# Kernel optimization log

Hardware: AMD Instinct MI355X
Metric: run time of the kernel (lower is better)

Reference implementation:

```python
import jax, jax.numpy as jnp
import numpy as np

NEG_BIG = -9e15  # matches torch's -9000000000000000.0 mask value


def _l2norm(x, eps=1e-12):
    # F.normalize(x, p=2, dim=1)
    n = jnp.sqrt(jnp.sum(x * x, axis=1, keepdims=True))
    return x / jnp.maximum(n, eps)


def _fusion_attribute(emb, att_emb, adj):
    # cosine similarity [N, M]
    sim = _l2norm(emb) @ _l2norm(att_emb).T
    sim = sim * adj
    # masked softmax over dim=1: zeros -> -9e15
    logits = jnp.where(sim != 0, sim, jnp.full_like(sim, NEG_BIG))
    attention = jax.nn.softmax(logits, axis=1)
    return attention @ att_emb


def setup_inputs() -> dict:
    key = jax.random.key(0)
    k1, k2, k3, k4 = jax.random.split(key, 4)
    U, I, D = 10000, 8000, 64
    users_emb = 0.1 * jax.random.normal(k1, (U, D), dtype=jnp.float32)  # init.normal_(std=0.1)
    items_emb = 0.1 * jax.random.normal(k2, (I, D), dtype=jnp.float32)
    Out_UserAttNets = (jax.random.uniform(k3, (U, I)) < 0.05).astype(jnp.float32)
    Out_ItemAttNets = (jax.random.uniform(k4, (I, U)) < 0.05).astype(jnp.float32)
    return {
        "num_users": U,
        "num_items": I,
        "users_emb": users_emb,
        "items_emb": items_emb,
        "Out_UserAttNets": Out_UserAttNets,
        "Out_ItemAttNets": Out_ItemAttNets,
    }


def reference(num_users, num_items, users_emb, items_emb, Out_UserAttNets, Out_ItemAttNets):
    out_useratt_emb = _fusion_attribute(users_emb, items_emb, Out_UserAttNets)
    out_itematt_emb = _fusion_attribute(items_emb, users_emb, Out_ItemAttNets)
    return (users_emb, items_emb, out_useratt_emb, out_itematt_emb)
```

## Files before the change

kernel.cpp:

```cpp
#include <hip/hip_runtime.h>
#include <math.h>

typedef float f32x4 __attribute__((ext_vector_type(4)));

#define SEGCAP 768

__global__ __launch_bounds__(256) void rinv_kernel(const float* __restrict__ users,
                                                   const float* __restrict__ items,
                                                   float* __restrict__ rinvU,
                                                   float* __restrict__ rinvI,
                                                   int U, int I) {
    int lane = threadIdx.x & 63;
    int row  = (blockIdx.x << 2) + (threadIdx.x >> 6);
    const float* src; float* dst;
    if (row < U) {
        src = users + (size_t)row * 64; dst = rinvU + row;
    } else {
        int r = row - U; if (r >= I) return;
        src = items + (size_t)r * 64; dst = rinvI + r;
    }
    float x = src[lane];
    float s = x * x;
#pragma unroll
    for (int off = 32; off; off >>= 1) s += __shfl_xor(s, off, 64);
    if (lane == 0) *dst = 1.0f / fmaxf(sqrtf(s), 1e-12f);
}

__global__ __launch_bounds__(256) void att_row_kernel(
    const float* __restrict__ users, const float* __restrict__ items,
    const float* __restrict__ adjU,  const float* __restrict__ adjI,
    const float* __restrict__ rinvU, const float* __restrict__ rinvI,
    float* __restrict__ outU, float* __restrict__ outI, int U, int I)
{
    __shared__ int cols_sh[4][SEGCAP];

    const int tid  = threadIdx.x;
    const int lane = tid & 63;
    const int wid  = tid >> 6;
    const int grow = (blockIdx.x << 2) + wid;
    if (grow >= U + I) return;

    const float* qemb; const float* kvemb; const float* adj;
    const float* rq;   const float* rk;    float* outp;
    int M, row;
    if (grow < U) {
        row = grow;     qemb = users; kvemb = items; adj = adjU;
        rq = rinvU; rk = rinvI; outp = outU; M = I;
    } else {
        row = grow - U; qemb = items; kvemb = users; adj = adjI;
        rq = rinvI; rk = rinvU; outp = outI; M = U;
    }
    const float* adjrow = adj + (size_t)row * M;

    int wcount = 0;
    const int M4 = M >> 2;
    const unsigned long long lt = (1ULL << lane) - 1ULL;
    for (int i4 = lane; i4 < M4; i4 += 64) {
        f32x4 a = __builtin_nontemporal_load((const f32x4*)adjrow + i4);
#pragma unroll
        for (int j = 0; j < 4; ++j) {
            bool pred = (a[j] != 0.0f);
            unsigned long long mask = __ballot(pred);
            if (pred) {
                int pos = wcount + __popcll(mask & lt);
                if (pos < SEGCAP) cols_sh[wid][pos] = (i4 << 2) + j;
            }
            wcount += __popcll(mask);
        }
    }
    wcount = __shfl(wcount, 0, 64);
    if (M & 3) {
        int idx = (M4 << 2) + lane;
        bool pred = (idx < M) && (adjrow[idx] != 0.0f);
        unsigned long long mask = __ballot(pred);
        if (pred) {
            int pos = wcount + __popcll(mask & lt);
            if (pos < SEGCAP) cols_sh[wid][pos] = idx;
        }
        wcount += __popcll(mask);
    }
    int cnt = wcount > SEGCAP ? SEGCAP : wcount;

    const int sub = lane & 15;
    const int grp = lane >> 4;

    const float rqv = rq[row];
    f32x4 q4 = ((const f32x4*)(qemb + (size_t)row * 64))[sub] * rqv;

    f32x4 acc = (f32x4){0.f, 0.f, 0.f, 0.f};
    float wsum = 0.f;
    const int* cp = cols_sh[wid];

    int i = grp;
    for (; i + 4 < cnt; i += 8) {
        int ca = cp[i], cb = cp[i + 4];
        float rka = rk[ca], rkb = rk[cb];
        f32x4 ra = ((const f32x4*)(kvemb + (size_t)ca * 64))[sub];
        f32x4 rb = ((const f32x4*)(kvemb + (size_t)cb * 64))[sub];
        float da = 0.f, db = 0.f;
#pragma unroll
        for (int c = 0; c < 4; ++c) {
            da = fmaf(q4[c], ra[c], da);
            db = fmaf(q4[c], rb[c], db);
        }
#pragma unroll
        for (int off = 1; off <= 8; off <<= 1) {
            da += __shfl_xor(da, off, 64);
            db += __shfl_xor(db, off, 64);
        }
        float sa = da * rka, sb = db * rkb;
        float wa = (sa != 0.0f) ? __expf(sa - 1.0f) : 0.0f;
        float wb = (sb != 0.0f) ? __expf(sb - 1.0f) : 0.0f;
#pragma unroll
        for (int c = 0; c < 4; ++c)
            acc[c] = fmaf(wa, ra[c], fmaf(wb, rb[c], acc[c]));
        if (sub == 0) wsum += wa + wb;
    }
    for (; i < cnt; i += 4) {
        int ca = cp[i];
        float rka = rk[ca];
        f32x4 ra = ((const f32x4*)(kvemb + (size_t)ca * 64))[sub];
        float da = 0.f;
#pragma unroll
        for (int c = 0; c < 4; ++c) da = fmaf(q4[c], ra[c], da);
#pragma unroll
        for (int off = 1; off <= 8; off <<= 1) da += __shfl_xor(da, off, 64);
        float sa = da * rka;
        float wa = (sa != 0.0f) ? __expf(sa - 1.0f) : 0.0f;
#pragma unroll
        for (int c = 0; c < 4; ++c) acc[c] = fmaf(wa, ra[c], acc[c]);
        if (sub == 0) wsum += wa;
    }

#pragma unroll
    for (int off = 16; off <= 32; off <<= 1) {
        wsum += __shfl_xor(wsum, off, 64);
#pragma unroll
        for (int c = 0; c < 4; ++c) acc[c] += __shfl_xor(acc[c], off, 64);
    }
    float den = __shfl(wsum, 0, 64);

    if (lane < 16) {
        float* orow = outp + (size_t)row * 64;
        if (den > 0.0f) {
            ((f32x4*)orow)[lane] = acc * (1.0f / den);
        } else {
            f32x4 m = (f32x4){0.f, 0.f, 0.f, 0.f};
            for (int r = 0; r < M; ++r)
                m += ((const f32x4*)(kvemb + (size_t)r * 64))[lane];
            ((f32x4*)orow)[lane] = m * (1.0f / (float)M);
        }
    }
}

extern "C" void kernel_launch(void* const* d_in, const int* in_sizes, int n_in,
                              void* d_out, int out_size, void* d_ws, size_t ws_size,
                              hipStream_t stream) {
    const float* users = (const float*)d_in[2];
    const float* items = (const float*)d_in[3];
    const float* adjU  = (const float*)d_in[4];
    const float* adjI  = (const float*)d_in[5];
    const int U = in_sizes[2] / 64;
    const int I = in_sizes[3] / 64;

    float* out   = (float*)d_out;
    float* rinvU = (float*)d_ws;
    float* rinvI = rinvU + U;

    hipMemcpyAsync(out, users, (size_t)U * 64 * sizeof(float),
                   hipMemcpyDeviceToDevice, stream);
    hipMemcpyAsync(out + (size_t)U * 64, items, (size_t)I * 64 * sizeof(float),
                   hipMemcpyDeviceToDevice, stream);

    rinv_kernel<<<(U + I + 3) / 4, 256, 0, stream>>>(users, items, rinvU, rinvI, U, I);

    float* outUatt = out + (size_t)(U + I) * 64;
    float* outIatt = outUatt + (size_t)U * 64;
    att_row_kernel<<<(U + I + 3) / 4, 256, 0, stream>>>(users, items, adjU, adjI,
                                                        rinvU, rinvI, outUatt, outIatt, U, I);
}
```

Baseline: 241.9 us.

## Split attention into per-direction persistent kernels with 4-way unrolled gather loop

Replaces the single combined kernel with one kernel per direction, launched twice. Each launch uses a grid-stride persistent loop over rows, capped at 2048 blocks. The gather/softmax loop is unrolled from 2 to 4 neighbors per iteration to put more independent loads in flight. The intent is to remove per-wave direction branching and improve memory-level parallelism. The cost is that the two launches now run in sequence and the unrolled loop uses more registers.

```diff
diff --git a/kernel.cpp b/kernel.cpp
--- a/kernel.cpp
+++ b/kernel.cpp
@@ -26,129 +26,129 @@
     if (lane == 0) *dst = 1.0f / fmaxf(sqrtf(s), 1e-12f);
 }
 
-__global__ __launch_bounds__(256) void att_row_kernel(
-    const float* __restrict__ users, const float* __restrict__ items,
-    const float* __restrict__ adjU,  const float* __restrict__ adjI,
-    const float* __restrict__ rinvU, const float* __restrict__ rinvI,
-    float* __restrict__ outU, float* __restrict__ outI, int U, int I)
+__global__ __launch_bounds__(256) void att_dir_kernel(
+    const float* __restrict__ qemb, const float* __restrict__ kvemb,
+    const float* __restrict__ adj,  const float* __restrict__ rq,
+    const float* __restrict__ rk,   float* __restrict__ outp,
+    int N, int M)
 {
     __shared__ int cols_sh[4][SEGCAP];
 
-    const int tid  = threadIdx.x;
-    const int lane = tid & 63;
-    const int wid  = tid >> 6;
-    const int grow = (blockIdx.x << 2) + wid;
-    if (grow >= U + I) return;
+    const int lane = threadIdx.x & 63;
+    const int wid  = threadIdx.x >> 6;
+    const int wave0   = (blockIdx.x << 2) + wid;
+    const int nwaves  = gridDim.x << 2;
 
-    const float* qemb; const float* kvemb; const float* adj;
-    const float* rq;   const float* rk;    float* outp;
-    int M, row;
-    if (grow < U) {
-        row = grow;     qemb = users; kvemb = items; adj = adjU;
-        rq = rinvU; rk = rinvI; outp = outU; M = I;
-    } else {
-        row = grow - U; qemb = items; kvemb = users; adj = adjI;
-        rq = rinvI; rk = rinvU; outp = outI; M = U;
-    }
-    const float* adjrow = adj + (size_t)row * M;
+    const int sub = lane & 15;
+    const int grp = lane >> 4;
+    const unsigned long long lt = (1ULL << lane) - 1ULL;
+    const int M4 = M >> 2;
+    const int* cp = cols_sh[wid];
 
-    int wcount = 0;
-    const int M4 = M >> 2;
-    const unsigned long long lt = (1ULL << lane) - 1ULL;
-    for (int i4 = lane; i4 < M4; i4 += 64) {
-        f32x4 a = __builtin_nontemporal_load((const f32x4*)adjrow + i4);
+    for (int row = wave0; row < N; row += nwaves) {
+        const float* adjrow = adj + (size_t)row * M;
+
+        int wcount = 0;
+        for (int i4 = lane; i4 < M4; i4 += 64) {
+            f32x4 a = __builtin_nontemporal_load((const f32x4*)adjrow + i4);
 #pragma unroll
-        for (int j = 0; j < 4; ++j) {
-            bool pred = (a[j] != 0.0f);
+            for (int j = 0; j < 4; ++j) {
+                bool pred = (a[j] != 0.0f);
+                unsigned long long mask = __ballot(pred);
+                if (pred) {
+                    int pos = wcount + __popcll(mask & lt);
+                    if (pos < SEGCAP) cols_sh[wid][pos] = (i4 << 2) + j;
+                }
+                wcount += __popcll(mask);
+            }
+        }
+        wcount = __shfl(wcount, 0, 64);
+        if (M & 3) {
+            int idx = (M4 << 2) + lane;
+            bool pred = (idx < M) && (adjrow[idx] != 0.0f);
             unsigned long long mask = __ballot(pred);
             if (pred) {
                 int pos = wcount + __popcll(mask & lt);
-                if (pos < SEGCAP) cols_sh[wid][pos] = (i4 << 2) + j;
+                if (pos < SEGCAP) cols_sh[wid][pos] = idx;
             }
             wcount += __popcll(mask);
         }
-    }
-    wcount = __shfl(wcount, 0, 64);
-    if (M & 3) {
-        int idx = (M4 << 2) + lane;
-        bool pred = (idx < M) && (adjrow[idx] != 0.0f);
-        unsigned long long mask = __ballot(pred);
-        if (pred) {
-            int pos = wcount + __popcll(mask & lt);
-            if (pos < SEGCAP) cols_sh[wid][pos] = idx;
+        int cnt = wcount > SEGCAP ? SEGCAP : wcount;
+
+        const float rqv = rq[row];
+        f32x4 q4 = ((const f32x4*)(qemb + (size_t)row * 64))[sub] * rqv;
+
+        f32x4 acc = (f32x4){0.f, 0.f, 0.f, 0.f};
+        float wsum = 0.f;
+
+        int i = grp;
+        for (; i + 12 < cnt; i += 16) {
+            int c0 = cp[i], c1 = cp[i + 4], c2 = cp[i + 8], c3 = cp[i + 12];
+            float k0 = rk[c0], k1 = rk[c1], k2 = rk[c2], k3 = rk[c3];
+            f32x4 r0 = ((const f32x4*)(kvemb + (size_t)c0 * 64))[sub];
+            f32x4 r1 = ((const f32x4*)(kvemb + (size_t)c1 * 64))[sub];
+            f32x4 r2 = ((const f32x4*)(kvemb + (size_t)c2 * 64))[sub];
+            f32x4 r3 = ((const f32x4*)(kvemb + (size_t)c3 * 64))[sub];
+            float d0 = 0.f, d1 = 0.f, d2 = 0.f, d3 = 0.f;
+#pragma unroll
+            for (int c = 0; c < 4; ++c) {
+                d0 = fmaf(q4[c], r0[c], d0);
+                d1 = fmaf(q4[c], r1[c], d1);
+                d2 = fmaf(q4[c], r2[c], d2);
+                d3 = fmaf(q4[c], r3[c], d3);
+            }
+#pragma unroll
+            for (int off = 1; off <= 8; off <<= 1) {
+                d0 += __shfl_xor(d0, off, 64);
+                d1 += __shfl_xor(d1, off, 64);
+                d2 += __shfl_xor(d2, off, 64);
+                d3 += __shfl_xor(d3, off, 64);
+            }
+            float s0 = d0 * k0, s1 = d1 * k1, s2 = d2 * k2, s3 = d3 * k3;
+            float w0 = (s0 != 0.0f) ? __expf(s0 - 1.0f) : 0.0f;
+            float w1 = (s1 != 0.0f) ? __expf(s1 - 1.0f) : 0.0f;
+            float w2 = (s2 != 0.0f) ? __expf(s2 - 1.0f) : 0.0f;
+            float w3 = (s3 != 0.0f) ? __expf(s3 - 1.0f) : 0.0f;
+#pragma unroll
+            for (int c = 0; c < 4; ++c)
+                acc[c] = fmaf(w0, r0[c], fmaf(w1, r1[c],
+                         fmaf(w2, r2[c], fmaf(w3, r3[c], acc[c]))));
+            if (sub == 0) wsum += (w0 + w1) + (w2 + w3);
         }
-        wcount += __popcll(mask);
-    }
-    int cnt = wcount > SEGCAP ? SEGCAP : wcount;
-
-    const int sub = lane & 15;
-    const int grp = lane >> 4;
-
-    const float rqv = rq[row];
-    f32x4 q4 = ((const f32x4*)(qemb + (size_t)row * 64))[sub] * rqv;
-
-    f32x4 acc = (f32x4){0.f, 0.f, 0.f, 0.f};
-    float wsum = 0.f;
-    const int* cp = cols_sh[wid];
-
-    int i = grp;
-    for (; i + 4 < cnt; i += 8) {
-        int ca = cp[i], cb = cp[i + 4];
-        float rka = rk[ca], rkb = rk[cb];
-        f32x4 ra = ((const f32x4*)(kvemb + (size_t)ca * 64))[sub];
-        f32x4 rb = ((const f32x4*)(kvemb + (size_t)cb * 64))[sub];
-        float da = 0.f, db = 0.f;
+        for (; i < cnt; i += 4) {
+            int c0 = cp[i];
+            float k0 = rk[c0];
+            f32x4 r0 = ((const f32x4*)(kvemb + (size_t)c0 * 64))[sub];
+            float d0 = 0.f;
 #pragma unroll
-        for (int c = 0; c < 4; ++c) {
-            da = fmaf(q4[c], ra[c], da);
-            db = fmaf(q4[c], rb[c], db);
+            for (int c = 0; c < 4; ++c) d0 = fmaf(q4[c], r0[c], d0);
+#pragma unroll
+            for (int off = 1; off <= 8; off <<= 1) d0 += __shfl_xor(d0, off, 64);
+            float s0 = d0 * k0;
+            float w0 = (s0 != 0.0f) ? __expf(s0 - 1.0f) : 0.0f;
+#pragma unroll
+            for (int c = 0; c < 4; ++c) acc[c] = fmaf(w0, r0[c], acc[c]);
+            if (sub == 0) wsum += w0;
         }
-#pragma unroll
-        for (int off = 1; off <= 8; off <<= 1) {
-            da += __shfl_xor(da, off, 64);
-            db += __shfl_xor(db, off, 64);
-        }
-        float sa = da * rka, sb = db * rkb;
-        float wa = (sa != 0.0f) ? __expf(sa - 1.0f) : 0.0f;
-        float wb = (sb != 0.0f) ? __expf(sb - 1.0f) : 0.0f;
-#pragma unroll
-        for (int c = 0; c < 4; ++c)
-            acc[c] = fmaf(wa, ra[c], fmaf(wb, rb[c], acc[c]));
-        if (sub == 0) wsum += wa + wb;
-    }
-    for (; i < cnt; i += 4) {
-        int ca = cp[i];
-        float rka = rk[ca];
-        f32x4 ra = ((const f32x4*)(kvemb + (size_t)ca * 64))[sub];
-        float da = 0.f;
-#pragma unroll
-        for (int c = 0; c < 4; ++c) da = fmaf(q4[c], ra[c], da);
-#pragma unroll
-        for (int off = 1; off <= 8; off <<= 1) da += __shfl_xor(da, off, 64);
-        float sa = da * rka;
-        float wa = (sa != 0.0f) ? __expf(sa - 1.0f) : 0.0f;
-#pragma unroll
-        for (int c = 0; c < 4; ++c) acc[c] = fmaf(wa, ra[c], acc[c]);
-        if (sub == 0) wsum += wa;
-    }
 
 #pragma unroll
-    for (int off = 16; off <= 32; off <<= 1) {
-        wsum += __shfl_xor(wsum, off, 64);
+        for (int off = 16; off <= 32; off <<= 1) {
+            wsum += __shfl_xor(wsum, off, 64);
 #pragma unroll
-        for (int c = 0; c < 4; ++c) acc[c] += __shfl_xor(acc[c], off, 64);
-    }
-    float den = __shfl(wsum, 0, 64);
+            for (int c = 0; c < 4; ++c) acc[c] += __shfl_xor(acc[c], off, 64);
+        }
+        float den = __shfl(wsum, 0, 64);
 
-    if (lane < 16) {
-        float* orow = outp + (size_t)row * 64;
-        if (den > 0.0f) {
-            ((f32x4*)orow)[lane] = acc * (1.0f / den);
-        } else {
-            f32x4 m = (f32x4){0.f, 0.f, 0.f, 0.f};
-            for (int r = 0; r < M; ++r)
-                m += ((const f32x4*)(kvemb + (size_t)r * 64))[lane];
-            ((f32x4*)orow)[lane] = m * (1.0f / (float)M);
+        if (lane < 16) {
+            float* orow = outp + (size_t)row * 64;
+            if (den > 0.0f) {
+                ((f32x4*)orow)[lane] = acc * (1.0f / den);
+            } else {
+                f32x4 m = (f32x4){0.f, 0.f, 0.f, 0.f};
+                for (int r = 0; r < M; ++r)
+                    m += ((const f32x4*)(kvemb + (size_t)r * 64))[lane];
+                ((f32x4*)orow)[lane] = m * (1.0f / (float)M);
+            }
         }
     }
 }
@@ -176,6 +176,11 @@
 
     float* outUatt = out + (size_t)(U + I) * 64;
     float* outIatt = outUatt + (size_t)U * 64;
-    att_row_kernel<<<(U + I + 3) / 4, 256, 0, stream>>>(users, items, adjU, adjI,
-                                                        rinvU, rinvI, outUatt, outIatt, U, I);
+
+    int gU = (U + 3) / 4; if (gU > 2048) gU = 2048;
+    int gI = (I + 3) / 4; if (gI > 2048) gI = 2048;
+    att_dir_kernel<<<gU, 256, 0, stream>>>(users, items, adjU, rinvU, rinvI,
+                                           outUatt, U, I);
+    att_dir_kernel<<<gI, 256, 0, stream>>>(items, users, adjI, rinvI, rinvU,
+                                           outIatt, I, U);
 }
```

Measured after the change: 261.4 us. 8.1% more time.
